# Kernel optimization log

Hardware: AMD Instinct MI355X
Metric: run time of the kernel (lower is better)

The kernel has to match this reference:

```python
import jax, jax.numpy as jnp
import numpy as np
from jax import lax

ALPHA = 0.2  # LeakyReLU negative slope


def setup_inputs() -> dict:
    key = jax.random.key(0)
    k1, k2, k3, k4, k5 = jax.random.split(key, 5)
    B, Cin, N, L = 16, 64, 1024, 12
    Cout, Kt = 64, 3
    inp = jax.random.normal(k1, (B, Cin, N, L), dtype=jnp.float32)
    adj = jax.random.normal(k2, (B, N, N), dtype=jnp.float32)
    w0 = jax.random.normal(k3, (Cout, Cin, 1, Kt), dtype=jnp.float32) * (1.0 / np.sqrt(Cin * Kt))
    b0 = jax.random.normal(k4, (Cout,), dtype=jnp.float32) * 0.01
    w1 = jax.random.normal(k5, (1, Cout * L, 1), dtype=jnp.float32) * (1.0 / np.sqrt(Cout * L))
    return {"input": inp, "adj": adj, "w0": w0, "b0": b0, "w1": w1}


def reference(input, adj, w0, b0, w1):
    # conv0: Conv2d(in,out,(1,Kt),padding=(0,1)) -> (B, Cout, N, L)
    x = lax.conv_general_dilated(
        input, w0, window_strides=(1, 1), padding=((0, 0), (1, 1)),
        dimension_numbers=("NCHW", "OIHW", "NCHW"))
    x = x + b0[None, :, None, None]
    B, C, N, L = x.shape
    # permute(0,1,3,2).view(B, C*L, N): channel-major over (C, L)
    x1 = jnp.transpose(x, (0, 1, 3, 2)).reshape(B, C * L, N)
    # conv1 (k=1, no bias) applied twice (original uses conv1 for both f_1 and f_2)
    f = jnp.einsum('bkn,k->bn', x1, w1[0, :, 0])  # (B, N)
    # logits[b,i,j] = f_1[b,0,j] + f_2[b,i,0]
    logits = f[:, None, :] + f[:, :, None]  # (B, N, N)
    z = jnp.where(logits >= 0, logits, ALPHA * logits) + adj
    attention = jax.nn.softmax(z, axis=-1)
    attention = jnp.swapaxes(attention, -1, -2)  # (B, N, N)
    h_prime = jnp.einsum('bcnl,bnq->bcql', x, attention)
    return h_prime, attention
```

## Files before the change

### kernel.cpp

```cpp
#include <hip/hip_runtime.h>
#include <stdint.h>

typedef unsigned short ushort_t;
typedef unsigned int uint_t;

#define B_SZ 16
#define CIN 64
#define COUT 64
#define N_SZ 1024
#define L_SZ 12
#define CL 768
#define NL 12288
#define PT 96
#define ALPHA 0.2f

typedef __bf16 bf16x8 __attribute__((ext_vector_type(8)));
typedef float floatx4 __attribute__((ext_vector_type(4)));
typedef _Float16 half8 __attribute__((ext_vector_type(8)));
typedef _Float16 half4 __attribute__((ext_vector_type(4)));

__device__ __forceinline__ ushort_t f2bf(float x) {
    uint_t u = __float_as_uint(x);
    u += 0x7fffu + ((u >> 16) & 1u);
    return (ushort_t)(u >> 16);
}
__device__ __forceinline__ float bf2f(ushort_t h) {
    return __uint_as_float(((uint_t)h) << 16);
}

#define ASYNC16(ldsp, gp)                                                \
    __builtin_amdgcn_global_load_lds(                                    \
        (const __attribute__((address_space(1))) void*)(gp),             \
        (__attribute__((address_space(3))) void*)(ldsp), 16, 0, 0)

__global__ __launch_bounds__(256, 4) void conv_mfma_kernel(
    const float* __restrict__ inp, const float* __restrict__ w0,
    const float* __restrict__ b0, const float* __restrict__ w1,
    ushort_t* __restrict__ Xt, float* __restrict__ fout)
{
    __shared__ _Float16 Bs[PT * 200];
    __shared__ float fredcol[PT];

    const int bx = blockIdx.x;
    const int b  = blockIdx.y;
    const int t  = threadIdx.x;
    const int lane = t & 63, w = t >> 6;
    const int rr = lane & 15, kc = lane >> 4;
    const int p0 = bx * PT;

    if (t < PT) fredcol[t] = 0.f;

    const float* ibase = inp + (size_t)b * CIN * NL;
    const half4 hz = (half4)(_Float16)0.f;
#pragma unroll
    for (int i = 0; i < 6; i++) {
        const int idx = i * 256 + t;
        const int p = idx % PT;
        const int cig = idx / PT;
        const int pg = p0 + p;
        const int l = pg % 12;
        const float* src = ibase + (size_t)(cig * 4) * NL + pg;
        half4 hv;
        hv[0] = (_Float16)src[0];
        hv[1] = (_Float16)src[NL];
        hv[2] = (_Float16)src[2 * NL];
        hv[3] = (_Float16)src[3 * NL];
        *(half4*)&Bs[p * 200 + 64 + cig * 4] = hv;
        if (p + 1 < PT) {
            half4 v0 = hv; if (l == 11) v0 = hz;
            *(half4*)&Bs[(p + 1) * 200 + cig * 4] = v0;
        }
        if (p >= 1) {
            half4 v2 = hv; if (l == 0) v2 = hz;
            *(half4*)&Bs[(p - 1) * 200 + 128 + cig * 4] = v2;
        }
    }
    if (t < 16) *(half4*)&Bs[0 * 200 + t * 4] = hz;
    else if (t < 32) *(half4*)&Bs[95 * 200 + 128 + (t - 16) * 4] = hz;

    const int co_r = w * 16 + rr;
    half8 af[6];
#pragma unroll
    for (int ch = 0; ch < 6; ch++) {
        const int kt = ch >> 1;
        const int ci0 = (ch & 1) * 32 + kc * 8;
        const float* wp = w0 + co_r * 192 + ci0 * 3 + kt;
#pragma unroll
        for (int e = 0; e < 8; e++) af[ch][e] = (_Float16)wp[e * 3];
    }

    __syncthreads();

    floatx4 acc[6];
#pragma unroll
    for (int fp = 0; fp < 6; fp++) acc[fp] = (floatx4)0.f;
#pragma unroll
    for (int fp = 0; fp < 6; fp++) {
        const _Float16* brow = &Bs[(fp * 16 + rr) * 200 + kc * 8];
#pragma unroll
        for (int ch = 0; ch < 6; ch++) {
            const half8 bf = *(const half8*)(brow + ch * 32);
            acc[fp] = __builtin_amdgcn_mfma_f32_16x16x32_f16(af[ch], bf, acc[fp], 0, 0, 0);
        }
    }

    float b0v[4];
#pragma unroll
    for (int r = 0; r < 4; r++) b0v[r] = b0[w * 16 + kc * 4 + r];

    ushort_t* XtB = Xt + (size_t)b * CL * N_SZ;
#pragma unroll
    for (int fp = 0; fp < 6; fp++) {
        const int pcol = fp * 16 + rr;
        const int pg = p0 + pcol;
        const int n = pg / 12;
        const int l = pg - n * 12;
        float fc = 0.f;
#pragma unroll
        for (int r = 0; r < 4; r++) {
            const int co = w * 16 + kc * 4 + r;
            const float x = acc[fp][r] + b0v[r];
            fc += x * w1[co * 12 + l];
            XtB[(size_t)(co * 12 + l) * N_SZ + n] = f2bf(x);
        }
        atomicAdd(&fredcol[pcol], fc);
    }
    __syncthreads();
    if (t < 8) {
        float s = 0.f;
#pragma unroll
        for (int j = 0; j < 12; j++) s += fredcol[t * 12 + j];
        fout[b * N_SZ + bx * 8 + t] = s;
    }
}

__global__ __launch_bounds__(256) void softmax_kernel(
    const float* __restrict__ adj, const float* __restrict__ f,
    ushort_t* __restrict__ Sb)
{
    __shared__ float smx[4], sms[4];
    const int i = blockIdx.x, b = blockIdx.y, t = threadIdx.x;
    const int lane = t & 63, wv = t >> 6;

    const float* frow = f + b * N_SZ;
    const float fi = frow[i];
    const float4 fj = *(const float4*)(frow + 4 * t);
    const float4 av = *(const float4*)(adj + ((size_t)b * N_SZ + i) * N_SZ + 4 * t);

    float z[4];
    z[0] = fi + fj.x; z[1] = fi + fj.y; z[2] = fi + fj.z; z[3] = fi + fj.w;
#pragma unroll
    for (int k = 0; k < 4; k++) z[k] = (z[k] >= 0.f) ? z[k] : ALPHA * z[k];
    z[0] += av.x; z[1] += av.y; z[2] += av.z; z[3] += av.w;

    float mx = fmaxf(fmaxf(z[0], z[1]), fmaxf(z[2], z[3]));
#pragma unroll
    for (int o = 32; o; o >>= 1) mx = fmaxf(mx, __shfl_xor(mx, o, 64));
    if (lane == 0) smx[wv] = mx;
    __syncthreads();
    mx = fmaxf(fmaxf(smx[0], smx[1]), fmaxf(smx[2], smx[3]));

    float e[4], s = 0.f;
#pragma unroll
    for (int k = 0; k < 4; k++) { e[k] = __expf(z[k] - mx); s += e[k]; }
#pragma unroll
    for (int o = 32; o; o >>= 1) s += __shfl_xor(s, o, 64);
    if (lane == 0) sms[wv] = s;
    __syncthreads();
    s = sms[0] + sms[1] + sms[2] + sms[3];
    const float inv = 1.0f / s;

    const uint_t p0 = (uint_t)f2bf(e[0] * inv) | ((uint_t)f2bf(e[1] * inv) << 16);
    const uint_t p1 = (uint_t)f2bf(e[2] * inv) | ((uint_t)f2bf(e[3] * inv) << 16);
    uint2 pk; pk.x = p0; pk.y = p1;
    *(uint2*)&Sb[((size_t)b * N_SZ + i) * N_SZ + 4 * t] = pk;
}

__global__ __launch_bounds__(256) void att_transpose_kernel(
    const ushort_t* __restrict__ Sb, float* __restrict__ att)
{
    __shared__ float T[64][65];
    const int b = blockIdx.z;
    const int i0 = blockIdx.x * 64, j0 = blockIdx.y * 64;
    const int t = threadIdx.x;

#pragma unroll
    for (int ph = 0; ph < 2; ph++) {
        const int idx = ph * 256 + t;
        const int r = idx >> 3, c8 = (idx & 7) * 8;
        const uint4 v = *(const uint4*)(Sb + ((size_t)b * N_SZ + i0 + r) * N_SZ + j0 + c8);
        T[r][c8 + 0] = bf2f((ushort_t)(v.x & 0xffff));
        T[r][c8 + 1] = bf2f((ushort_t)(v.x >> 16));
        T[r][c8 + 2] = bf2f((ushort_t)(v.y & 0xffff));
        T[r][c8 + 3] = bf2f((ushort_t)(v.y >> 16));
        T[r][c8 + 4] = bf2f((ushort_t)(v.z & 0xffff));
        T[r][c8 + 5] = bf2f((ushort_t)(v.z >> 16));
        T[r][c8 + 6] = bf2f((ushort_t)(v.w & 0xffff));
        T[r][c8 + 7] = bf2f((ushort_t)(v.w >> 16));
    }
    __syncthreads();
#pragma unroll
    for (int ph = 0; ph < 4; ph++) {
        const int idx = ph * 256 + t;
        const int jr = idx >> 4, i4 = (idx & 15) * 4;
        float4 o;
        o.x = T[i4 + 0][jr]; o.y = T[i4 + 1][jr];
        o.z = T[i4 + 2][jr]; o.w = T[i4 + 3][jr];
        *(float4*)(att + ((size_t)b * N_SZ + j0 + jr) * N_SZ + i0 + i4) = o;
    }
}

__global__ __launch_bounds__(256) void gemm2_kernel(
    const ushort_t* __restrict__ Sb, const ushort_t* __restrict__ Xt,
    float* __restrict__ out)
{
    __shared__ ushort_t As[1024 * 8];
    __shared__ ushort_t Bs[1024 * 8];
    const int b = blockIdx.z;
    const int m0 = blockIdx.x * 128, q0 = blockIdx.y * 128;
    const int t = threadIdx.x;
    const int lane = t & 63, wv = t >> 6;
    const int wq = wv >> 1, wm = wv & 1;
    const int kc = lane >> 4, rr = lane & 15;

    const ushort_t* Sbase = Sb + (size_t)b * N_SZ * N_SZ;
    const ushort_t* Xbase = Xt + (size_t)b * CL * N_SZ;

    floatx4 acc[4][4];
#pragma unroll
    for (int i = 0; i < 4; i++)
#pragma unroll
        for (int j = 0; j < 4; j++) acc[i][j] = (floatx4)0.f;

    for (int k0 = 0; k0 < N_SZ; k0 += 64) {
        __syncthreads();
#pragma unroll
        for (int c = 0; c < 4; c++) {
            const int u = c * 256 + t;
            const int r = u & 127, kcs = u >> 7;
            ASYNC16(&As[u * 8], Sbase + (size_t)(q0 + r) * N_SZ + k0 + kcs * 8);
            ASYNC16(&Bs[u * 8], Xbase + (size_t)(m0 + r) * N_SZ + k0 + kcs * 8);
        }
        __syncthreads();

#pragma unroll
        for (int kk = 0; kk < 2; kk++) {
            bf16x8 af[4], bfr[4];
#pragma unroll
            for (int i = 0; i < 4; i++) {
                af[i]  = *(const bf16x8*)&As[((kk * 4 + kc) * 128 + wq * 64 + i * 16 + rr) * 8];
                bfr[i] = *(const bf16x8*)&Bs[((kk * 4 + kc) * 128 + wm * 64 + i * 16 + rr) * 8];
            }
#pragma unroll
            for (int i = 0; i < 4; i++)
#pragma unroll
                for (int j = 0; j < 4; j++)
                    acc[i][j] = __builtin_amdgcn_mfma_f32_16x16x32_bf16(
                        af[i], bfr[j], acc[i][j], 0, 0, 0);
        }
    }

#pragma unroll
    for (int j = 0; j < 4; j++) {
        const int m = m0 + wm * 64 + j * 16 + rr;
        const int co = m / 12, l = m - co * 12;
        float* ob = out + (size_t)(b * COUT + co) * (N_SZ * L_SZ) + l;
#pragma unroll
        for (int i = 0; i < 4; i++) {
            const int q = q0 + wq * 64 + i * 16 + kc * 4;
#pragma unroll
            for (int r2 = 0; r2 < 4; r2++)
                ob[(size_t)(q + r2) * 12] = acc[i][j][r2];
        }
    }
}

extern "C" void kernel_launch(void* const* d_in, const int* in_sizes, int n_in,
                              void* d_out, int out_size, void* d_ws, size_t ws_size,
                              hipStream_t stream)
{
    const float* inp = (const float*)d_in[0];
    const float* adj = (const float*)d_in[1];
    const float* w0  = (const float*)d_in[2];
    const float* b0  = (const float*)d_in[3];
    const float* w1  = (const float*)d_in[4];

    float* hprime = (float*)d_out;
    float* att    = hprime + (size_t)B_SZ * COUT * N_SZ * L_SZ;

    char* ws = (char*)d_ws;
    ushort_t* Xt = (ushort_t*)ws;
    ushort_t* Sb = (ushort_t*)(ws + (size_t)25165824);
    float*    fw = (float*)(ws + (size_t)25165824 + 33554432);

    conv_mfma_kernel<<<dim3(NL / PT, B_SZ), 256, 0, stream>>>(inp, w0, b0, w1, Xt, fw);
    softmax_kernel<<<dim3(N_SZ, B_SZ), 256, 0, stream>>>(adj, fw, Sb);
    att_transpose_kernel<<<dim3(N_SZ / 64, N_SZ / 64, B_SZ), 256, 0, stream>>>(Sb, att);
    gemm2_kernel<<<dim3(CL / 128, N_SZ / 128, B_SZ), 256, 0, stream>>>(Sb, Xt, hprime);
}
```

Baseline: 394.0 us.

## Make conv blocks persistent over eight tiles to reuse loaded weights

The conv kernel now launches 16 blocks per batch instead of 128. Each block loops over eight 96-position tiles, reusing the A-fragment weights, bias and w1 values it keeps in registers, and resets the shared reduction buffer between tiles. This cuts the repeated weight loads and per-block setup, but leaves only one block per batch column. Occupancy is much lower and each block's load, MFMA and store phases run one after another with no overlap, so memory latency may be poorly hidden.

```diff
diff --git a/kernel.cpp b/kernel.cpp
--- a/kernel.cpp
+++ b/kernel.cpp
@@ -11,7 +11,6 @@
 #define L_SZ 12
 #define CL 768
 #define NL 12288
-#define PT 96
 #define ALPHA 0.2f
 
 typedef __bf16 bf16x8 __attribute__((ext_vector_type(8)));
@@ -38,43 +37,17 @@
     const float* __restrict__ b0, const float* __restrict__ w1,
     ushort_t* __restrict__ Xt, float* __restrict__ fout)
 {
-    __shared__ _Float16 Bs[PT * 200];
-    __shared__ float fredcol[PT];
+    __shared__ _Float16 Bs[96 * 200];
+    __shared__ float fredcol[96];
 
     const int bx = blockIdx.x;
     const int b  = blockIdx.y;
     const int t  = threadIdx.x;
     const int lane = t & 63, w = t >> 6;
     const int rr = lane & 15, kc = lane >> 4;
-    const int p0 = bx * PT;
-
-    if (t < PT) fredcol[t] = 0.f;
-
-    const float* ibase = inp + (size_t)b * CIN * NL;
     const half4 hz = (half4)(_Float16)0.f;
-#pragma unroll
-    for (int i = 0; i < 6; i++) {
-        const int idx = i * 256 + t;
-        const int p = idx % PT;
-        const int cig = idx / PT;
-        const int pg = p0 + p;
-        const int l = pg % 12;
-        const float* src = ibase + (size_t)(cig * 4) * NL + pg;
-        half4 hv;
-        hv[0] = (_Float16)src[0];
-        hv[1] = (_Float16)src[NL];
-        hv[2] = (_Float16)src[2 * NL];
-        hv[3] = (_Float16)src[3 * NL];
-        *(half4*)&Bs[p * 200 + 64 + cig * 4] = hv;
-        if (p + 1 < PT) {
-            half4 v0 = hv; if (l == 11) v0 = hz;
-            *(half4*)&Bs[(p + 1) * 200 + cig * 4] = v0;
-        }
-        if (p >= 1) {
-            half4 v2 = hv; if (l == 0) v2 = hz;
-            *(half4*)&Bs[(p - 1) * 200 + 128 + cig * 4] = v2;
-        }
-    }
+
+    if (t < 96) fredcol[t] = 0.f;
     if (t < 16) *(half4*)&Bs[0 * 200 + t * 4] = hz;
     else if (t < 32) *(half4*)&Bs[95 * 200 + 128 + (t - 16) * 4] = hz;
 
@@ -89,48 +62,84 @@
         for (int e = 0; e < 8; e++) af[ch][e] = (_Float16)wp[e * 3];
     }
 
-    __syncthreads();
-
-    floatx4 acc[6];
-#pragma unroll
-    for (int fp = 0; fp < 6; fp++) acc[fp] = (floatx4)0.f;
-#pragma unroll
-    for (int fp = 0; fp < 6; fp++) {
-        const _Float16* brow = &Bs[(fp * 16 + rr) * 200 + kc * 8];
-#pragma unroll
-        for (int ch = 0; ch < 6; ch++) {
-            const half8 bf = *(const half8*)(brow + ch * 32);
-            acc[fp] = __builtin_amdgcn_mfma_f32_16x16x32_f16(af[ch], bf, acc[fp], 0, 0, 0);
-        }
-    }
-
-    float b0v[4];
-#pragma unroll
-    for (int r = 0; r < 4; r++) b0v[r] = b0[w * 16 + kc * 4 + r];
-
+    float b0v[4], w1v[4][12];
+#pragma unroll
+    for (int r = 0; r < 4; r++) {
+        b0v[r] = b0[w * 16 + kc * 4 + r];
+#pragma unroll
+        for (int l = 0; l < 12; l++) w1v[r][l] = w1[(w * 16 + kc * 4 + r) * 12 + l];
+    }
+
+    const float* ibase = inp + (size_t)b * CIN * NL;
     ushort_t* XtB = Xt + (size_t)b * CL * N_SZ;
-#pragma unroll
-    for (int fp = 0; fp < 6; fp++) {
-        const int pcol = fp * 16 + rr;
-        const int pg = p0 + pcol;
-        const int n = pg / 12;
-        const int l = pg - n * 12;
-        float fc = 0.f;
-#pragma unroll
-        for (int r = 0; r < 4; r++) {
-            const int co = w * 16 + kc * 4 + r;
-            const float x = acc[fp][r] + b0v[r];
-            fc += x * w1[co * 12 + l];
-            XtB[(size_t)(co * 12 + l) * N_SZ + n] = f2bf(x);
-        }
-        atomicAdd(&fredcol[pcol], fc);
-    }
-    __syncthreads();
-    if (t < 8) {
-        float s = 0.f;
-#pragma unroll
-        for (int j = 0; j < 12; j++) s += fredcol[t * 12 + j];
-        fout[b * N_SZ + bx * 8 + t] = s;
+
+#pragma unroll 1
+    for (int g = 0; g < 8; g++) {
+        const int p0 = bx * 768 + g * 96;
+
+#pragma unroll
+        for (int i = 0; i < 6; i++) {
+            const int idx = i * 256 + t;
+            const int p = idx % 96;
+            const int cig = idx / 96;
+            const int l = p % 12;
+            const float* src = ibase + (size_t)(cig * 4) * NL + p0 + p;
+            half4 hv;
+            hv[0] = (_Float16)src[0];
+            hv[1] = (_Float16)src[NL];
+            hv[2] = (_Float16)src[2 * NL];
+            hv[3] = (_Float16)src[3 * NL];
+            *(half4*)&Bs[p * 200 + 64 + cig * 4] = hv;
+            if (p + 1 < 96) {
+                half4 v0 = hv; if (l == 11) v0 = hz;
+                *(half4*)&Bs[(p + 1) * 200 + cig * 4] = v0;
+            }
+            if (p >= 1) {
+                half4 v2 = hv; if (l == 0) v2 = hz;
+                *(half4*)&Bs[(p - 1) * 200 + 128 + cig * 4] = v2;
+            }
+        }
+        __syncthreads();
+
+        floatx4 acc[6];
+#pragma unroll
+        for (int fp = 0; fp < 6; fp++) acc[fp] = (floatx4)0.f;
+#pragma unroll
+        for (int fp = 0; fp < 6; fp++) {
+            const _Float16* brow = &Bs[(fp * 16 + rr) * 200 + kc * 8];
+#pragma unroll
+            for (int ch = 0; ch < 6; ch++) {
+                const half8 bf = *(const half8*)(brow + ch * 32);
+                acc[fp] = __builtin_amdgcn_mfma_f32_16x16x32_f16(af[ch], bf, acc[fp], 0, 0, 0);
+            }
+        }
+
+#pragma unroll
+        for (int fp = 0; fp < 6; fp++) {
+            const int pcol = fp * 16 + rr;
+            const int pg = p0 + pcol;
+            const int n = pg / 12;
+            const int l = pcol % 12;
+            float fc = 0.f;
+#pragma unroll
+            for (int r = 0; r < 4; r++) {
+                const int co = w * 16 + kc * 4 + r;
+                const float x = acc[fp][r] + b0v[r];
+                fc += x * w1v[r][l];
+                XtB[(size_t)(co * 12 + l) * N_SZ + n] = f2bf(x);
+            }
+            atomicAdd(&fredcol[pcol], fc);
+        }
+        __syncthreads();
+
+        if (t < 8) {
+            float s = 0.f;
+#pragma unroll
+            for (int j = 0; j < 12; j++) s += fredcol[t * 12 + j];
+            fout[b * N_SZ + bx * 64 + g * 8 + t] = s;
+#pragma unroll
+            for (int j = 0; j < 12; j++) fredcol[t * 12 + j] = 0.f;
+        }
     }
 }
 
@@ -293,7 +302,7 @@
     ushort_t* Sb = (ushort_t*)(ws + (size_t)25165824);
     float*    fw = (float*)(ws + (size_t)25165824 + 33554432);
 
-    conv_mfma_kernel<<<dim3(NL / PT, B_SZ), 256, 0, stream>>>(inp, w0, b0, w1, Xt, fw);
+    conv_mfma_kernel<<<dim3(16, B_SZ), 256, 0, stream>>>(inp, w0, b0, w1, Xt, fw);
     softmax_kernel<<<dim3(N_SZ, B_SZ), 256, 0, stream>>>(adj, fw, Sb);
     att_transpose_kernel<<<dim3(N_SZ / 64, N_SZ / 64, B_SZ), 256, 0, stream>>>(Sb, att);
     gemm2_kernel<<<dim3(CL / 128, N_SZ / 128, B_SZ), 256, 0, stream>>>(Sb, Xt, hprime);
```

Result: slower. 454.0 us (+15.2%).
